# Optimization experiments

Measured on AMD Instinct MI355X. Metric: run time of the kernel, lower is better.

The kernel has to match this reference:

```python
import jax, jax.numpy as jnp
import numpy as np


def setup_inputs() -> dict:
    key = jax.random.key(0)
    k1, k2, k3, k4 = jax.random.split(key, 4)
    B, N, F, H, O = 4, 2048, 256, 8, 256
    nodes = jax.random.normal(k1, (B, N, F), dtype=jnp.float32)
    W_heads = jax.random.normal(k2, (H, F, F), dtype=jnp.float32) * (1.0 / np.sqrt(F))
    W_out = jax.random.normal(k3, (H * F, O), dtype=jnp.float32) * (1.0 / np.sqrt(H * F))
    bias = jax.random.normal(k4, (O,), dtype=jnp.float32) * 0.02
    return {"nodes": nodes, "W_heads": W_heads, "W_out": W_out, "bias": bias}


def reference(nodes, W_heads, W_out, bias):
    # nodes: [B,N,F]; W_heads: [H,F,F]; W_out: [H*F,O]; bias: [O]
    B, N, F = nodes.shape
    H = W_heads.shape[0]
    norm = 1.0 / jnp.sqrt(jnp.asarray(F, dtype=nodes.dtype))
    # per-head bilinear scores: (x @ W_h) @ x^T  -> [B,H,N,N]
    xw = jnp.einsum('bnf,hfg->bhng', nodes, W_heads)
    scores = jnp.einsum('bhng,bmg->bhnm', xw, nodes) * norm
    att = jax.nn.softmax(scores, axis=-1)
    # messages: att @ x (V = input nodes) -> [B,H,N,F]
    msgs = jnp.einsum('bhnm,bmf->bhnf', att, nodes)
    # concat heads along feature axis (head 0 first) -> [B,N,H*F]
    msgs = msgs.transpose(0, 2, 1, 3).reshape(B, N, H * F)
    return jnp.matmul(msgs, W_out) + bias
```

## Files before the change

### kernel.cpp

```cpp
#include <hip/hip_runtime.h>
#include <hip/hip_bf16.h>

#define B_ 4
#define N_ 2048
#define F_ 256
#define H_ 8
#define O_ 256

#define SCALE_QK 0.09016844005556021f

typedef __attribute__((ext_vector_type(8))) short short8;
typedef __attribute__((ext_vector_type(4))) short s16x4;
typedef __attribute__((ext_vector_type(4))) float f32x4;
typedef __attribute__((ext_vector_type(4))) unsigned int u32x4;

static __device__ __forceinline__ float bf2f(short u) {
    unsigned int x = ((unsigned int)(unsigned short)u) << 16;
    return __builtin_bit_cast(float, x);
}
static __device__ __forceinline__ short f2bf(float f) {
    unsigned int x = __builtin_bit_cast(unsigned int, f);
    unsigned int lsb = (x >> 16) & 1u;
    x += 0x7fffu + lsb;
    return (short)(x >> 16);
}
static __device__ __forceinline__ unsigned int pkbf(float a, float b) {
    return (unsigned int)(unsigned short)f2bf(a) |
           ((unsigned int)(unsigned short)f2bf(b) << 16);
}

static __device__ __forceinline__ void gld16(const short* g, short* l) {
    __builtin_amdgcn_global_load_lds(
        (const __attribute__((address_space(1))) void*)g,
        (__attribute__((address_space(3))) void*)l, 16, 0, 0);
}

__global__ __launch_bounds__(256) void cvtT_kernel(const float* __restrict__ src,
                                                   short* __restrict__ dst,
                                                   int R, int C) {
    __shared__ short tile[32][33];
    src += (size_t)blockIdx.z * R * C;
    dst += (size_t)blockIdx.z * R * C;
    int tx = threadIdx.x, ty = threadIdx.y;
    int c0 = blockIdx.x * 32, r0 = blockIdx.y * 32;
#pragma unroll
    for (int j = 0; j < 4; j++) {
        int r = r0 + ty + j * 8;
        tile[ty + j * 8][tx] = f2bf(src[(size_t)r * C + c0 + tx]);
    }
    __syncthreads();
#pragma unroll
    for (int j = 0; j < 4; j++) {
        int c = c0 + ty + j * 8;
        dst[(size_t)c * R + r0 + tx] = tile[tx][ty + j * 8];
    }
}

__global__ __launch_bounds__(256) void cvt_kernel(const float* __restrict__ src,
                                                  short* __restrict__ dst, int n) {
    int i = blockIdx.x * 256 + threadIdx.x;
    if (n >= 2048) {
        size_t base = (size_t)i * 8;
#pragma unroll
        for (int j = 0; j < 8; j++) dst[base + j] = f2bf(src[base + j]);
    } else if (i < n) {
        dst[i] = f2bf(src[i]);
    }
}

template <int NCT>
__device__ __forceinline__ void gemm64_bt(const short* __restrict__ A, int lda,
                                          const short* __restrict__ Bt, int ldb,
                                          float* __restrict__ C, int ldc,
                                          int K, const short* __restrict__ bias) {
    __shared__ short sA[64][72];
    __shared__ short sB[NCT * 16][72];
    int tid = threadIdx.x;
    int w = tid >> 6, l = tid & 63, lq = l & 15, quad = l >> 4;
    f32x4 acc[NCT];
#pragma unroll
    for (int i = 0; i < NCT; i++) acc[i] = (f32x4)(0.f);

    for (int kb = 0; kb < K; kb += 64) {
        __syncthreads();
#pragma unroll
        for (int i = 0; i < 2; i++) {
            int idx = tid + i * 256; int r = idx >> 3, c = (idx & 7) * 8;
            *(short8*)&sA[r][c] = *(const short8*)&A[(size_t)r * lda + kb + c];
        }
#pragma unroll
        for (int i = 0; i < NCT / 2; i++) {
            int idx = tid + i * 256; int r = idx >> 3, c = (idx & 7) * 8;
            *(short8*)&sB[r][c] = *(const short8*)&Bt[(size_t)r * ldb + kb + c];
        }
        __syncthreads();
#pragma unroll
        for (int kk = 0; kk < 2; kk++) {
            short8 af = *(const short8*)&sA[w * 16 + lq][kk * 32 + quad * 8];
#pragma unroll
            for (int ct = 0; ct < NCT; ct++) {
                short8 bf = *(const short8*)&sB[ct * 16 + lq][kk * 32 + quad * 8];
                acc[ct] = __builtin_amdgcn_mfma_f32_16x16x32_bf16(af, bf, acc[ct], 0, 0, 0);
            }
        }
    }
#pragma unroll
    for (int ct = 0; ct < NCT; ct++) {
        int col = ct * 16 + lq;
        float bv = bias ? bf2f(bias[col]) : 0.f;
#pragma unroll
        for (int r = 0; r < 4; r++) {
            int row = w * 16 + quad * 4 + r;
            C[(size_t)row * ldc + col] = acc[ct][r] + bv;
        }
    }
}

__global__ __launch_bounds__(256) void out_kernel(const short* __restrict__ msgs,
                                                  const short* __restrict__ WoutT,
                                                  const short* __restrict__ bias,
                                                  float* __restrict__ out) {
    int mt = blockIdx.x, nt = blockIdx.y;
    gemm64_bt<4>(msgs + (size_t)mt * 64 * (H_ * F_), H_ * F_,
                 WoutT + (size_t)nt * 64 * (H_ * F_), H_ * F_,
                 out + (size_t)mt * 64 * O_ + nt * 64, O_,
                 H_ * F_, bias + nt * 64);
}


#define STAGE_KV(KT, KVF, KVTF) do {                                         \
    _Pragma("unroll")                                                        \
    for (int i_ = 0; i_ < 4; i_++) {                                         \
        int rk_ = w * 8 + i_ * 2 + (l >> 5);                                 \
        int bk_ = (l & 31) ^ (rk_ & 31);                                     \
        gld16(&Xb[(size_t)((KT) * 64 + rk_) * F_ + bk_ * 8],                 \
              &KVF[(w * 8 + i_ * 2) * 256]);                                 \
        int rt_ = w * 32 + i_ * 8 + (l >> 3);                                \
        int bt_ = (l & 7) ^ (rt_ & 7);                                       \
        gld16(&XTb[(size_t)rt_ * N_ + (KT) * 64 + bt_ * 8],                  \
              &KVTF[(w * 32 + i_ * 8) * 64]);                                \
    }                                                                        \
} while (0)

#define COMPUTE_KT(KVF, KVTF) do {                                           \
    f32x4 sacc[4];                                                           \
    _Pragma("unroll")                                                        \
    for (int ct = 0; ct < 4; ct++) sacc[ct] = (f32x4)(0.f);                  \
    _Pragma("unroll")                                                        \
    for (int kk = 0; kk < 8; kk++) {                                         \
        _Pragma("unroll")                                                    \
        for (int ct = 0; ct < 4; ct++) {                                     \
            int arow = ct * 16 + lq;                                         \
            int ab = (kk * 4 + quad) ^ (arow & 31);                          \
            short8 af = *(const short8*)&KVF[arow * 256 + ab * 8];           \
            sacc[ct] = __builtin_amdgcn_mfma_f32_16x16x32_bf16(af, aq[kk], sacc[ct], 0, 0, 0); \
        }                                                                    \
    }                                                                        \
    float mx = -INFINITY;                                                    \
    _Pragma("unroll")                                                        \
    for (int ct = 0; ct < 4; ct++)                                           \
        _Pragma("unroll")                                                    \
        for (int r_ = 0; r_ < 4; r_++) mx = fmaxf(mx, sacc[ct][r_]);         \
    mx = fmaxf(mx, __shfl_xor(mx, 16));                                      \
    mx = fmaxf(mx, __shfl_xor(mx, 32));                                      \
    float mn = fmaxf(m_q, mx);                                               \
    float alpha = exp2f(m_q - mn);                                           \
    m_q = mn;                                                                \
    float pv[4][4]; float s_ = 0.f;                                          \
    _Pragma("unroll")                                                        \
    for (int ct = 0; ct < 4; ct++)                                           \
        _Pragma("unroll")                                                    \
        for (int r_ = 0; r_ < 4; r_++) {                                     \
            pv[ct][r_] = exp2f(sacc[ct][r_] - mn);                           \
            s_ += pv[ct][r_];                                                \
        }                                                                    \
    s_ += __shfl_xor(s_, 16);                                                \
    s_ += __shfl_xor(s_, 32);                                                \
    l_q = l_q * alpha + s_;                                                  \
    if (!__all(alpha == 1.0f)) {                                             \
        _Pragma("unroll")                                                    \
        for (int ct = 0; ct < 16; ct++)                                      \
            _Pragma("unroll")                                                \
            for (int r_ = 0; r_ < 4; r_++) oacc[ct][r_] *= alpha;            \
    }                                                                        \
    unsigned int w2[4][2];                                                   \
    _Pragma("unroll")                                                        \
    for (int ct = 0; ct < 4; ct++) {                                         \
        w2[ct][0] = pkbf(pv[ct][0], pv[ct][1]);                              \
        w2[ct][1] = pkbf(pv[ct][2], pv[ct][3]);                              \
    }                                                                        \
    int sl0 = (2 * (quad & 1)) * 16 + lq;                                    \
    int sl1 = sl0 + 16;                                                      \
    bool hi = (quad >> 1) != 0;                                              \
    short8 pfrag[2];                                                         \
    _Pragma("unroll")                                                        \
    for (int kk = 0; kk < 2; kk++) {                                         \
        unsigned int u0 = __shfl((int)w2[2 * kk][0], sl0);                   \
        unsigned int u1 = __shfl((int)w2[2 * kk][1], sl0);                   \
        unsigned int u2 = __shfl((int)w2[2 * kk][0], sl1);                   \
        unsigned int u3 = __shfl((int)w2[2 * kk][1], sl1);                   \
        unsigned int v0 = __shfl((int)w2[2 * kk + 1][0], sl0);               \
        unsigned int v1 = __shfl((int)w2[2 * kk + 1][1], sl0);               \
        unsigned int v2 = __shfl((int)w2[2 * kk + 1][0], sl1);               \
        unsigned int v3 = __shfl((int)w2[2 * kk + 1][1], sl1);               \
        u32x4 pk = { hi ? v0 : u0, hi ? v1 : u1, hi ? v2 : u2, hi ? v3 : u3 }; \
        pfrag[kk] = __builtin_bit_cast(short8, pk);                          \
    }                                                                        \
    _Pragma("unroll")                                                        \
    for (int ct = 0; ct < 16; ct++) {                                        \
        int arow = ct * 16 + lq;                                             \
        short8 a0 = *(const short8*)&KVTF[arow * 64 + ((quad) ^ (arow & 7)) * 8]; \
        short8 a1 = *(const short8*)&KVTF[arow * 64 + ((4 + quad) ^ (arow & 7)) * 8]; \
        oacc[ct] = __builtin_amdgcn_mfma_f32_16x16x32_bf16(a0, pfrag[0], oacc[ct], 0, 0, 0); \
        oacc[ct] = __builtin_amdgcn_mfma_f32_16x16x32_bf16(a1, pfrag[1], oacc[ct], 0, 0, 0); \
    }                                                                        \
} while (0)

__global__ __launch_bounds__(512) void attn_kernel(const short* __restrict__ X,
                                                   const short* __restrict__ WhT,
                                                   const short* __restrict__ XT,
                                                   short* __restrict__ msgs) {
    __shared__ short kvfA[64 * 256];
    __shared__ short kvfB[64 * 256];
    __shared__ short kvTfA[256 * 64];
    __shared__ short kvTfB[256 * 64];

    int qt = blockIdx.x, bh = blockIdx.y, b = bh >> 3, h = bh & 7;
    int tid = threadIdx.x, w = tid >> 6, l = tid & 63, lq = l & 15, quad = l >> 4;
    int q0 = qt * 128;

    const short* Xb  = X  + (size_t)b * N_ * F_;
    const short* XTb = XT + (size_t)b * F_ * N_;
    const short* Whh = WhT + (size_t)h * F_ * F_;

    f32x4 oacc[16];
    short8 aq[8];

#pragma unroll
    for (int i = 0; i < 16; i++) oacc[i] = (f32x4)(0.f);
    {
        short* xdst = (w < 4) ? kvfA : kvfB;
        int wl = w & 3;
#pragma unroll
        for (int i = 0; i < 8; i++) {
            int r = wl * 16 + i * 2 + (l >> 5);
            int bb = (l & 31) ^ (r & 31);
            gld16(&Xb[(size_t)(q0 + ((w >> 2) * 64) + r) * F_ + bb * 8],
                  &xdst[(wl * 16 + i * 2) * 256]);
        }
    }
    const short* xsrc = (w < 4) ? kvfA : kvfB;
#pragma unroll 1
    for (int kb = 0; kb < 4; kb++) {
        __syncthreads();
#pragma unroll
        for (int i = 0; i < 4; i++) {
            int rt = w * 32 + i * 8 + (l >> 3);
            int bt = (l & 7) ^ (rt & 7);
            gld16(&Whh[(size_t)rt * F_ + kb * 64 + bt * 8], &kvTfA[(w * 32 + i * 8) * 64]);
        }
        __syncthreads();
#pragma unroll
        for (int kk = 0; kk < 2; kk++) {
            int arow = (w & 3) * 16 + lq;
            int ab = (kb * 8 + kk * 4 + quad) ^ (arow & 31);
            short8 af = *(const short8*)&xsrc[arow * 256 + ab * 8];
#pragma unroll
            for (int ct = 0; ct < 16; ct++) {
                int brow = ct * 16 + lq;
                int bb = (kk * 4 + quad) ^ (brow & 7);
                short8 bf = *(const short8*)&kvTfA[brow * 64 + bb * 8];
                oacc[ct] = __builtin_amdgcn_mfma_f32_16x16x32_bf16(af, bf, oacc[ct], 0, 0, 0);
            }
        }
    }
    __syncthreads();
    {
        short* qdst = (w < 4) ? kvTfA : kvTfB;
#pragma unroll
        for (int ct = 0; ct < 16; ct++) {
#pragma unroll
            for (int r = 0; r < 4; r++) {
                int row = (w & 3) * 16 + quad * 4 + r;
                int col = ct * 16 + lq;
                int pb = (col >> 3) ^ (row & 31);
                qdst[row * 256 + pb * 8 + (col & 7)] = f2bf(oacc[ct][r] * SCALE_QK);
            }
        }
        __syncthreads();
#pragma unroll
        for (int kk = 0; kk < 8; kk++) {
            int row = (w & 3) * 16 + lq;
            int ab = (kk * 4 + quad) ^ (row & 31);
            aq[kk] = *(const short8*)&qdst[row * 256 + ab * 8];
        }
    }
    __syncthreads();

#pragma unroll
    for (int i = 0; i < 16; i++) oacc[i] = (f32x4)(0.f);
    float m_q = -INFINITY, l_q = 0.f;

    STAGE_KV(0, kvfA, kvTfA);
    __syncthreads();

#pragma unroll 1
    for (int kt2 = 0; kt2 < 16; kt2++) {
        STAGE_KV(2 * kt2 + 1, kvfB, kvTfB);
        COMPUTE_KT(kvfA, kvTfA);
        __syncthreads();
        STAGE_KV((2 * kt2 + 2) & 31, kvfA, kvTfA);
        COMPUTE_KT(kvfB, kvTfB);
        __syncthreads();
    }

    float inv = 1.f / l_q;
    short* Mout = msgs + (size_t)(b * N_ + q0 + w * 16 + lq) * (H_ * F_) + h * F_;
#pragma unroll
    for (int ct = 0; ct < 16; ct++) {
        s16x4 v4 = { f2bf(oacc[ct][0] * inv), f2bf(oacc[ct][1] * inv),
                     f2bf(oacc[ct][2] * inv), f2bf(oacc[ct][3] * inv) };
        *(s16x4*)&Mout[ct * 16 + quad * 4] = v4;
    }
}

extern "C" void kernel_launch(void* const* d_in, const int* in_sizes, int n_in,
                              void* d_out, int out_size, void* d_ws, size_t ws_size,
                              hipStream_t stream) {
    const float* nodes = (const float*)d_in[0];
    const float* Wh    = (const float*)d_in[1];
    const float* Wout  = (const float*)d_in[2];
    const float* bias  = (const float*)d_in[3];
    float* out = (float*)d_out;

    char* ws = (char*)d_ws;
    short* msgs   = (short*)(ws);
    short* WhT    = (short*)(ws + 33554432);
    short* WoutT  = (short*)(ws + 34603008);
    short* XT     = (short*)(ws + 35651584);
    short* Xbf    = (short*)(ws + 39845888);
    short* biasbf = (short*)(ws + 44040192);

    dim3 tblk(32, 8, 1);
    hipLaunchKernelGGL(cvtT_kernel, dim3(8, 8, 8),  tblk, 0, stream, Wh,    WhT,   256,  256);
    hipLaunchKernelGGL(cvtT_kernel, dim3(8, 64, 1), tblk, 0, stream, Wout,  WoutT, 2048, 256);
    hipLaunchKernelGGL(cvtT_kernel, dim3(8, 64, 4), tblk, 0, stream, nodes, XT,    2048, 256);
    hipLaunchKernelGGL(cvt_kernel,  dim3(1024), dim3(256), 0, stream, nodes, Xbf, 2097152);
    hipLaunchKernelGGL(cvt_kernel,  dim3(1),    dim3(256), 0, stream, bias, biasbf, 256);

    hipLaunchKernelGGL(attn_kernel, dim3(16, 32), dim3(512), 0, stream, Xbf, WhT, XT, msgs);
    hipLaunchKernelGGL(out_kernel,  dim3(128, 4), dim3(256), 0, stream, msgs, WoutT, biasbf, out);
}
```

Measured before the change: 295.5 us.

## Process two 16-row query tiles per wave in attention kernel, halving block threads

Each wave now handles two sets of 16 query rows (128 queries per block with 4 waves instead of 8), reusing every K/V LDS fragment load for two MFMA streams in both the score and PV phases. The goal is to halve LDS read traffic per MFMA and cut synchronisation overhead per unit of work. In exchange, accumulator registers double (oacc is now 2x16 f32x4 plus 2x8 aq fragments), which may lower occupancy or spill. Staging loops do twice as many loads per thread to cover the same tile.

```diff
diff --git a/kernel.cpp b/kernel.cpp
--- a/kernel.cpp
+++ b/kernel.cpp
@@ -130,22 +130,24 @@
 
 #define STAGE_KV(KT, KVF, KVTF) do {                                         \
     _Pragma("unroll")                                                        \
-    for (int i_ = 0; i_ < 4; i_++) {                                         \
-        int rk_ = w * 8 + i_ * 2 + (l >> 5);                                 \
+    for (int i_ = 0; i_ < 8; i_++) {                                         \
+        int rk_ = w * 16 + i_ * 2 + (l >> 5);                                \
         int bk_ = (l & 31) ^ (rk_ & 31);                                     \
         gld16(&Xb[(size_t)((KT) * 64 + rk_) * F_ + bk_ * 8],                 \
-              &KVF[(w * 8 + i_ * 2) * 256]);                                 \
-        int rt_ = w * 32 + i_ * 8 + (l >> 3);                                \
+              &KVF[(w * 16 + i_ * 2) * 256]);                                \
+        int rt_ = w * 64 + i_ * 8 + (l >> 3);                                \
         int bt_ = (l & 7) ^ (rt_ & 7);                                       \
         gld16(&XTb[(size_t)rt_ * N_ + (KT) * 64 + bt_ * 8],                  \
-              &KVTF[(w * 32 + i_ * 8) * 64]);                                \
+              &KVTF[(w * 64 + i_ * 8) * 64]);                                \
     }                                                                        \
 } while (0)
 
 #define COMPUTE_KT(KVF, KVTF) do {                                           \
-    f32x4 sacc[4];                                                           \
-    _Pragma("unroll")                                                        \
-    for (int ct = 0; ct < 4; ct++) sacc[ct] = (f32x4)(0.f);                  \
+    f32x4 sacc[2][4];                                                        \
+    _Pragma("unroll")                                                        \
+    for (int m_ = 0; m_ < 2; m_++)                                           \
+        _Pragma("unroll")                                                    \
+        for (int ct = 0; ct < 4; ct++) sacc[m_][ct] = (f32x4)(0.f);          \
     _Pragma("unroll")                                                        \
     for (int kk = 0; kk < 8; kk++) {                                         \
         _Pragma("unroll")                                                    \
@@ -153,70 +155,79 @@
             int arow = ct * 16 + lq;                                         \
             int ab = (kk * 4 + quad) ^ (arow & 31);                          \
             short8 af = *(const short8*)&KVF[arow * 256 + ab * 8];           \
-            sacc[ct] = __builtin_amdgcn_mfma_f32_16x16x32_bf16(af, aq[kk], sacc[ct], 0, 0, 0); \
+            sacc[0][ct] = __builtin_amdgcn_mfma_f32_16x16x32_bf16(af, aq[0][kk], sacc[0][ct], 0, 0, 0); \
+            sacc[1][ct] = __builtin_amdgcn_mfma_f32_16x16x32_bf16(af, aq[1][kk], sacc[1][ct], 0, 0, 0); \
         }                                                                    \
     }                                                                        \
-    float mx = -INFINITY;                                                    \
-    _Pragma("unroll")                                                        \
-    for (int ct = 0; ct < 4; ct++)                                           \
-        _Pragma("unroll")                                                    \
-        for (int r_ = 0; r_ < 4; r_++) mx = fmaxf(mx, sacc[ct][r_]);         \
-    mx = fmaxf(mx, __shfl_xor(mx, 16));                                      \
-    mx = fmaxf(mx, __shfl_xor(mx, 32));                                      \
-    float mn = fmaxf(m_q, mx);                                               \
-    float alpha = exp2f(m_q - mn);                                           \
-    m_q = mn;                                                                \
-    float pv[4][4]; float s_ = 0.f;                                          \
-    _Pragma("unroll")                                                        \
-    for (int ct = 0; ct < 4; ct++)                                           \
-        _Pragma("unroll")                                                    \
-        for (int r_ = 0; r_ < 4; r_++) {                                     \
-            pv[ct][r_] = exp2f(sacc[ct][r_] - mn);                           \
-            s_ += pv[ct][r_];                                                \
+    float alpha[2];                                                          \
+    short8 pfrag[2][2];                                                      \
+    _Pragma("unroll")                                                        \
+    for (int m_ = 0; m_ < 2; m_++) {                                         \
+        float mx = -INFINITY;                                                \
+        _Pragma("unroll")                                                    \
+        for (int ct = 0; ct < 4; ct++)                                       \
+            _Pragma("unroll")                                                \
+            for (int r_ = 0; r_ < 4; r_++) mx = fmaxf(mx, sacc[m_][ct][r_]); \
+        mx = fmaxf(mx, __shfl_xor(mx, 16));                                  \
+        mx = fmaxf(mx, __shfl_xor(mx, 32));                                  \
+        float mn = fmaxf(m_q[m_], mx);                                       \
+        alpha[m_] = exp2f(m_q[m_] - mn);                                     \
+        m_q[m_] = mn;                                                        \
+        float pv[4][4]; float s_ = 0.f;                                      \
+        _Pragma("unroll")                                                    \
+        for (int ct = 0; ct < 4; ct++)                                       \
+            _Pragma("unroll")                                                \
+            for (int r_ = 0; r_ < 4; r_++) {                                 \
+                pv[ct][r_] = exp2f(sacc[m_][ct][r_] - mn);                   \
+                s_ += pv[ct][r_];                                            \
+            }                                                                \
+        s_ += __shfl_xor(s_, 16);                                            \
+        s_ += __shfl_xor(s_, 32);                                            \
+        l_q[m_] = l_q[m_] * alpha[m_] + s_;                                  \
+        unsigned int w2[4][2];                                               \
+        _Pragma("unroll")                                                    \
+        for (int ct = 0; ct < 4; ct++) {                                     \
+            w2[ct][0] = pkbf(pv[ct][0], pv[ct][1]);                          \
+            w2[ct][1] = pkbf(pv[ct][2], pv[ct][3]);                          \
         }                                                                    \
-    s_ += __shfl_xor(s_, 16);                                                \
-    s_ += __shfl_xor(s_, 32);                                                \
-    l_q = l_q * alpha + s_;                                                  \
-    if (!__all(alpha == 1.0f)) {                                             \
-        _Pragma("unroll")                                                    \
-        for (int ct = 0; ct < 16; ct++)                                      \
+        int sl0 = (2 * (quad & 1)) * 16 + lq;                                \
+        int sl1 = sl0 + 16;                                                  \
+        bool hi = (quad >> 1) != 0;                                          \
+        _Pragma("unroll")                                                    \
+        for (int kk = 0; kk < 2; kk++) {                                     \
+            unsigned int u0 = __shfl((int)w2[2 * kk][0], sl0);               \
+            unsigned int u1 = __shfl((int)w2[2 * kk][1], sl0);               \
+            unsigned int u2 = __shfl((int)w2[2 * kk][0], sl1);               \
+            unsigned int u3 = __shfl((int)w2[2 * kk][1], sl1);               \
+            unsigned int v0 = __shfl((int)w2[2 * kk + 1][0], sl0);           \
+            unsigned int v1 = __shfl((int)w2[2 * kk + 1][1], sl0);           \
+            unsigned int v2 = __shfl((int)w2[2 * kk + 1][0], sl1);           \
+            unsigned int v3 = __shfl((int)w2[2 * kk + 1][1], sl1);           \
+            u32x4 pk = { hi ? v0 : u0, hi ? v1 : u1, hi ? v2 : u2, hi ? v3 : u3 }; \
+            pfrag[m_][kk] = __builtin_bit_cast(short8, pk);                  \
+        }                                                                    \
+    }                                                                        \
+    if (!__all(alpha[0] == 1.0f && alpha[1] == 1.0f)) {                      \
+        _Pragma("unroll")                                                    \
+        for (int m_ = 0; m_ < 2; m_++)                                       \
             _Pragma("unroll")                                                \
-            for (int r_ = 0; r_ < 4; r_++) oacc[ct][r_] *= alpha;            \
-    }                                                                        \
-    unsigned int w2[4][2];                                                   \
-    _Pragma("unroll")                                                        \
-    for (int ct = 0; ct < 4; ct++) {                                         \
-        w2[ct][0] = pkbf(pv[ct][0], pv[ct][1]);                              \
-        w2[ct][1] = pkbf(pv[ct][2], pv[ct][3]);                              \
-    }                                                                        \
-    int sl0 = (2 * (quad & 1)) * 16 + lq;                                    \
-    int sl1 = sl0 + 16;                                                      \
-    bool hi = (quad >> 1) != 0;                                              \
-    short8 pfrag[2];                                                         \
-    _Pragma("unroll")                                                        \
-    for (int kk = 0; kk < 2; kk++) {                                         \
-        unsigned int u0 = __shfl((int)w2[2 * kk][0], sl0);                   \
-        unsigned int u1 = __shfl((int)w2[2 * kk][1], sl0);                   \
-        unsigned int u2 = __shfl((int)w2[2 * kk][0], sl1);                   \
-        unsigned int u3 = __shfl((int)w2[2 * kk][1], sl1);                   \
-        unsigned int v0 = __shfl((int)w2[2 * kk + 1][0], sl0);               \
-        unsigned int v1 = __shfl((int)w2[2 * kk + 1][1], sl0);               \
-        unsigned int v2 = __shfl((int)w2[2 * kk + 1][0], sl1);               \
-        unsigned int v3 = __shfl((int)w2[2 * kk + 1][1], sl1);               \
-        u32x4 pk = { hi ? v0 : u0, hi ? v1 : u1, hi ? v2 : u2, hi ? v3 : u3 }; \
-        pfrag[kk] = __builtin_bit_cast(short8, pk);                          \
+            for (int ct = 0; ct < 16; ct++)                                  \
+                _Pragma("unroll")                                            \
+                for (int r_ = 0; r_ < 4; r_++) oacc[m_][ct][r_] *= alpha[m_]; \
     }                                                                        \
     _Pragma("unroll")                                                        \
     for (int ct = 0; ct < 16; ct++) {                                        \
         int arow = ct * 16 + lq;                                             \
         short8 a0 = *(const short8*)&KVTF[arow * 64 + ((quad) ^ (arow & 7)) * 8]; \
         short8 a1 = *(const short8*)&KVTF[arow * 64 + ((4 + quad) ^ (arow & 7)) * 8]; \
-        oacc[ct] = __builtin_amdgcn_mfma_f32_16x16x32_bf16(a0, pfrag[0], oacc[ct], 0, 0, 0); \
-        oacc[ct] = __builtin_amdgcn_mfma_f32_16x16x32_bf16(a1, pfrag[1], oacc[ct], 0, 0, 0); \
+        oacc[0][ct] = __builtin_amdgcn_mfma_f32_16x16x32_bf16(a0, pfrag[0][0], oacc[0][ct], 0, 0, 0); \
+        oacc[0][ct] = __builtin_amdgcn_mfma_f32_16x16x32_bf16(a1, pfrag[0][1], oacc[0][ct], 0, 0, 0); \
+        oacc[1][ct] = __builtin_amdgcn_mfma_f32_16x16x32_bf16(a0, pfrag[1][0], oacc[1][ct], 0, 0, 0); \
+        oacc[1][ct] = __builtin_amdgcn_mfma_f32_16x16x32_bf16(a1, pfrag[1][1], oacc[1][ct], 0, 0, 0); \
     }                                                                        \
 } while (0)
 
-__global__ __launch_bounds__(512) void attn_kernel(const short* __restrict__ X,
+__global__ __launch_bounds__(256) void attn_kernel(const short* __restrict__ X,
                                                    const short* __restrict__ WhT,
                                                    const short* __restrict__ XT,
                                                    short* __restrict__ msgs) {
@@ -233,73 +244,74 @@
     const short* XTb = XT + (size_t)b * F_ * N_;
     const short* Whh = WhT + (size_t)h * F_ * F_;
 
-    f32x4 oacc[16];
-    short8 aq[8];
-
-#pragma unroll
-    for (int i = 0; i < 16; i++) oacc[i] = (f32x4)(0.f);
-    {
-        short* xdst = (w < 4) ? kvfA : kvfB;
-        int wl = w & 3;
-#pragma unroll
-        for (int i = 0; i < 8; i++) {
-            int r = wl * 16 + i * 2 + (l >> 5);
-            int bb = (l & 31) ^ (r & 31);
-            gld16(&Xb[(size_t)(q0 + ((w >> 2) * 64) + r) * F_ + bb * 8],
-                  &xdst[(wl * 16 + i * 2) * 256]);
-        }
-    }
-    const short* xsrc = (w < 4) ? kvfA : kvfB;
+    f32x4 oacc[2][16];
+    short8 aq[2][8];
+
+#pragma unroll
+    for (int m = 0; m < 2; m++)
+#pragma unroll
+        for (int i = 0; i < 16; i++) oacc[m][i] = (f32x4)(0.f);
+#pragma unroll
+    for (int i = 0; i < 8; i++) {
+        int r = w * 16 + i * 2 + (l >> 5);
+        int bb = (l & 31) ^ (r & 31);
+        gld16(&Xb[(size_t)(q0 + r) * F_ + bb * 8],       &kvfA[(w * 16 + i * 2) * 256]);
+        gld16(&Xb[(size_t)(q0 + 64 + r) * F_ + bb * 8],  &kvfB[(w * 16 + i * 2) * 256]);
+    }
 #pragma unroll 1
     for (int kb = 0; kb < 4; kb++) {
         __syncthreads();
 #pragma unroll
-        for (int i = 0; i < 4; i++) {
-            int rt = w * 32 + i * 8 + (l >> 3);
+        for (int i = 0; i < 8; i++) {
+            int rt = w * 64 + i * 8 + (l >> 3);
             int bt = (l & 7) ^ (rt & 7);
-            gld16(&Whh[(size_t)rt * F_ + kb * 64 + bt * 8], &kvTfA[(w * 32 + i * 8) * 64]);
+            gld16(&Whh[(size_t)rt * F_ + kb * 64 + bt * 8], &kvTfA[(w * 64 + i * 8) * 64]);
         }
         __syncthreads();
 #pragma unroll
         for (int kk = 0; kk < 2; kk++) {
-            int arow = (w & 3) * 16 + lq;
+            int arow = w * 16 + lq;
             int ab = (kb * 8 + kk * 4 + quad) ^ (arow & 31);
-            short8 af = *(const short8*)&xsrc[arow * 256 + ab * 8];
+            short8 af0 = *(const short8*)&kvfA[arow * 256 + ab * 8];
+            short8 af1 = *(const short8*)&kvfB[arow * 256 + ab * 8];
 #pragma unroll
             for (int ct = 0; ct < 16; ct++) {
                 int brow = ct * 16 + lq;
                 int bb = (kk * 4 + quad) ^ (brow & 7);
                 short8 bf = *(const short8*)&kvTfA[brow * 64 + bb * 8];
-                oacc[ct] = __builtin_amdgcn_mfma_f32_16x16x32_bf16(af, bf, oacc[ct], 0, 0, 0);
+                oacc[0][ct] = __builtin_amdgcn_mfma_f32_16x16x32_bf16(af0, bf, oacc[0][ct], 0, 0, 0);
+                oacc[1][ct] = __builtin_amdgcn_mfma_f32_16x16x32_bf16(af1, bf, oacc[1][ct], 0, 0, 0);
             }
         }
     }
     __syncthreads();
-    {
-        short* qdst = (w < 4) ? kvTfA : kvTfB;
-#pragma unroll
-        for (int ct = 0; ct < 16; ct++) {
-#pragma unroll
-            for (int r = 0; r < 4; r++) {
-                int row = (w & 3) * 16 + quad * 4 + r;
-                int col = ct * 16 + lq;
-                int pb = (col >> 3) ^ (row & 31);
-                qdst[row * 256 + pb * 8 + (col & 7)] = f2bf(oacc[ct][r] * SCALE_QK);
-            }
-        }
-        __syncthreads();
-#pragma unroll
-        for (int kk = 0; kk < 8; kk++) {
-            int row = (w & 3) * 16 + lq;
-            int ab = (kk * 4 + quad) ^ (row & 31);
-            aq[kk] = *(const short8*)&qdst[row * 256 + ab * 8];
-        }
-    }
-    __syncthreads();
-
-#pragma unroll
-    for (int i = 0; i < 16; i++) oacc[i] = (f32x4)(0.f);
-    float m_q = -INFINITY, l_q = 0.f;
+#pragma unroll
+    for (int ct = 0; ct < 16; ct++) {
+#pragma unroll
+        for (int r = 0; r < 4; r++) {
+            int row = w * 16 + quad * 4 + r;
+            int col = ct * 16 + lq;
+            int pb = (col >> 3) ^ (row & 31);
+            kvTfA[row * 256 + pb * 8 + (col & 7)] = f2bf(oacc[0][ct][r] * SCALE_QK);
+            kvTfB[row * 256 + pb * 8 + (col & 7)] = f2bf(oacc[1][ct][r] * SCALE_QK);
+        }
+    }
+    __syncthreads();
+#pragma unroll
+    for (int kk = 0; kk < 8; kk++) {
+        int row = w * 16 + lq;
+        int ab = (kk * 4 + quad) ^ (row & 31);
+        aq[0][kk] = *(const short8*)&kvTfA[row * 256 + ab * 8];
+        aq[1][kk] = *(const short8*)&kvTfB[row * 256 + ab * 8];
+    }
+    __syncthreads();
+
+#pragma unroll
+    for (int m = 0; m < 2; m++)
+#pragma unroll
+        for (int i = 0; i < 16; i++) oacc[m][i] = (f32x4)(0.f);
+    float m_q[2] = {-INFINITY, -INFINITY};
+    float l_q[2] = {0.f, 0.f};
 
     STAGE_KV(0, kvfA, kvTfA);
     __syncthreads();
@@ -314,13 +326,16 @@
         __syncthreads();
     }
 
-    float inv = 1.f / l_q;
-    short* Mout = msgs + (size_t)(b * N_ + q0 + w * 16 + lq) * (H_ * F_) + h * F_;
-#pragma unroll
-    for (int ct = 0; ct < 16; ct++) {
-        s16x4 v4 = { f2bf(oacc[ct][0] * inv), f2bf(oacc[ct][1] * inv),
-                     f2bf(oacc[ct][2] * inv), f2bf(oacc[ct][3] * inv) };
-        *(s16x4*)&Mout[ct * 16 + quad * 4] = v4;
+#pragma unroll
+    for (int m = 0; m < 2; m++) {
+        float inv = 1.f / l_q[m];
+        short* Mout = msgs + (size_t)(b * N_ + q0 + m * 64 + w * 16 + lq) * (H_ * F_) + h * F_;
+#pragma unroll
+        for (int ct = 0; ct < 16; ct++) {
+            s16x4 v4 = { f2bf(oacc[m][ct][0] * inv), f2bf(oacc[m][ct][1] * inv),
+                         f2bf(oacc[m][ct][2] * inv), f2bf(oacc[m][ct][3] * inv) };
+            *(s16x4*)&Mout[ct * 16 + quad * 4] = v4;
+        }
     }
 }
 
@@ -348,6 +363,6 @@
     hipLaunchKernelGGL(cvt_kernel,  dim3(1024), dim3(256), 0, stream, nodes, Xbf, 2097152);
     hipLaunchKernelGGL(cvt_kernel,  dim3(1),    dim3(256), 0, stream, bias, biasbf, 256);
 
-    hipLaunchKernelGGL(attn_kernel, dim3(16, 32), dim3(512), 0, stream, Xbf, WhT, XT, msgs);
+    hipLaunchKernelGGL(attn_kernel, dim3(16, 32), dim3(256), 0, stream, Xbf, WhT, XT, msgs);
     hipLaunchKernelGGL(out_kernel,  dim3(128, 4), dim3(256), 0, stream, msgs, WoutT, biasbf, out);
 }
```

After: 369.2 us. +24.9%, slower.
